# Performance work log

Measured on AMD Instinct MI355X. Metric: run time of the kernel, lower is better.

## Reference

```python
import jax, jax.numpy as jnp
import numpy as np


def setup_inputs() -> dict:
    key = jax.random.key(0)
    k1, k2 = jax.random.split(key)
    imgs = jax.random.normal(k1, (4, 16, 64, 64), dtype=jnp.float32)
    kernel = jax.random.normal(k2, (16, 16, 5, 5), dtype=jnp.float32)
    return {"imgs": imgs, "kernel": kernel, "stride": 1, "padding": 2}


def reference(imgs, kernel, stride, padding):
    # Tropical-max (T+) semifield convolution (morphological dilation):
    #   multiply = add, add_reduce = max, zero = -inf, kind='conv' (kernel flipped)
    B, C, H, W = imgs.shape
    O, _, kH, kW = kernel.shape
    x = jnp.pad(imgs, ((0, 0), (0, 0), (padding, padding), (padding, padding)),
                constant_values=-jnp.inf)
    # kind='conv' flips the kernel spatially
    k = kernel[:, :, ::-1, ::-1]
    # im2col-style window extraction: [B, C*kH*kW, oH, oW], channel-major (C, kH, kW)
    patches = jax.lax.conv_general_dilated_patches(
        x, (kH, kW), (stride, stride), padding="VALID")
    oH, oW = patches.shape[2], patches.shape[3]
    win = patches.reshape(B, 1, C, kH, kW, oH, oW)
    w = k.reshape(1, O, C, kH, kW, 1, 1)
    # broadcast semifield multiply (add), then semifield reduce (max) over (C, kH, kW)
    out = jnp.max(win + w, axis=(2, 3, 4))  # [B, O, oH, oW]
    return out
```

## Files before the change

### kernel.cpp

```cpp
#include <hip/hip_runtime.h>
#include <math.h>


#define NEG_INF (-__builtin_inff())

#define PW 68
#define PPLANE (PW * PW)

__global__ __launch_bounds__(256) void pad_kernel(
        const float* __restrict__ img, float* __restrict__ pad) {
    const int idx   = blockIdx.x * 256 + threadIdx.x;
    const int plane = idx / PPLANE;
    const int rem   = idx % PPLANE;
    const int py    = rem / PW;
    const int px    = rem % PW;
    const int yy = py - 2, xx = px - 2;
    float v = NEG_INF;
    if ((unsigned)yy < 64u && (unsigned)xx < 64u)
        v = img[(plane << 12) + (yy << 6) + xx];
    pad[idx] = v;
}

__global__ __launch_bounds__(256, 4) void bconv_kernel(
        const float* __restrict__ pad,
        const float* __restrict__ kern,
        float* __restrict__ out) {
    const int x  = threadIdx.x & 63;
    const int w  = __builtin_amdgcn_readfirstlane(threadIdx.x >> 6);
    const int y  = blockIdx.x;
    const int og = blockIdx.y;
    const int b  = blockIdx.z;
    const int o0 = og * 4;
    const int c0 = w * 4;

    __shared__ float red[4][4][64];

    float acc0 = NEG_INF, acc1 = NEG_INF, acc2 = NEG_INF, acc3 = NEG_INF;

#pragma unroll
    for (int cc = 0; cc < 4; ++cc) {
        const int c = c0 + cc;
        const float* __restrict__ pl = pad + (b * 16 + c) * PPLANE + y * PW + x;

        float v[25];
#pragma unroll
        for (int i = 0; i < 5; ++i)
#pragma unroll
            for (int j = 0; j < 5; ++j)
                v[i * 5 + j] = pl[i * PW + j];

#define ACC_O(oo, A)                                                     \
        {                                                                \
            const float* __restrict__ kp = kern + ((o0 + oo) * 16 + c) * 25; \
            float kw[25];                                                \
            _Pragma("unroll")                                            \
            for (int t = 0; t < 25; ++t) kw[t] = kp[t];                  \
            _Pragma("unroll")                                            \
            for (int g = 0; g < 5; ++g) {                                \
                float t0 = v[g * 5 + 0] + kw[24 - (g * 5 + 0)];          \
                float t1 = v[g * 5 + 1] + kw[24 - (g * 5 + 1)];          \
                float t2 = v[g * 5 + 2] + kw[24 - (g * 5 + 2)];          \
                float t3 = v[g * 5 + 3] + kw[24 - (g * 5 + 3)];          \
                float t4 = v[g * 5 + 4] + kw[24 - (g * 5 + 4)];          \
                A = fmaxf(A, fmaxf(t0, t1));                             \
                A = fmaxf(A, fmaxf(t2, t3));                             \
                A = fmaxf(A, t4);                                        \
            }                                                            \
        }
        ACC_O(0, acc0)
        ACC_O(1, acc1)
        ACC_O(2, acc2)
        ACC_O(3, acc3)
#undef ACC_O
    }

    red[w][0][x] = acc0;
    red[w][1][x] = acc1;
    red[w][2][x] = acc2;
    red[w][3][x] = acc3;
    __syncthreads();

    const int oo = threadIdx.x >> 6;
    float r = fmaxf(fmaxf(red[0][oo][x], red[1][oo][x]),
                    fmaxf(red[2][oo][x], red[3][oo][x]));
    out[(((b * 16 + o0 + oo) << 6) + y) * 64 + x] = r;
}

extern "C" void kernel_launch(void* const* d_in, const int* in_sizes, int n_in,
                              void* d_out, int out_size, void* d_ws, size_t ws_size,
                              hipStream_t stream) {
    const float* img  = (const float*)d_in[0];
    const float* kern = (const float*)d_in[1];
    float* out = (float*)d_out;
    float* pad = (float*)d_ws;
    (void)in_sizes; (void)n_in; (void)out_size; (void)ws_size;

    hipLaunchKernelGGL(pad_kernel, dim3(1156), dim3(256), 0, stream, img, pad);

    dim3 grid(64, 4, 4);
    hipLaunchKernelGGL(bconv_kernel, grid, dim3(256), 0, stream, pad, kern, out);
}
```

Measured before the change: 66.40 us.

## Vectorize pad and window loads, double block size to 8 channel-split waves

The pad kernel now writes a float4 per thread, so it launches a quarter as many blocks. The conv kernel runs 512 threads with 8 waves, each handling 2 input channels instead of 4, and reduces across 8 partial results in shared memory. Window rows are read with unaligned 4-wide vector loads, the adds use 2-wide vector types, and the channel loop is no longer unrolled. The aim is more parallelism and fewer load instructions, at the cost of a larger reduction and half the threads sitting idle in the final step.

```diff
diff --git a/kernel.cpp b/kernel.cpp
--- a/kernel.cpp
+++ b/kernel.cpp
@@ -3,25 +3,34 @@
 
 
 #define NEG_INF (-__builtin_inff())
-
 #define PW 68
 #define PPLANE (PW * PW)
 
+typedef float f32x2  __attribute__((ext_vector_type(2)));
+typedef float f32x4u __attribute__((ext_vector_type(4), aligned(4)));
+
 __global__ __launch_bounds__(256) void pad_kernel(
         const float* __restrict__ img, float* __restrict__ pad) {
-    const int idx   = blockIdx.x * 256 + threadIdx.x;
-    const int plane = idx / PPLANE;
-    const int rem   = idx % PPLANE;
-    const int py    = rem / PW;
-    const int px    = rem % PW;
-    const int yy = py - 2, xx = px - 2;
-    float v = NEG_INF;
-    if ((unsigned)yy < 64u && (unsigned)xx < 64u)
-        v = img[(plane << 12) + (yy << 6) + xx];
-    pad[idx] = v;
+    const int idx4  = blockIdx.x * 256 + threadIdx.x;
+    const int plane = idx4 / 1156;
+    const int r4    = idx4 - plane * 1156;
+    const int py    = r4 / 17;
+    const int px0   = (r4 - py * 17) * 4;
+    const int yy    = py - 2;
+    const bool yok  = (unsigned)yy < 64u;
+    const float* src = img + (plane << 12) + ((yok ? yy : 0) << 6);
+    float o[4];
+#pragma unroll
+    for (int t = 0; t < 4; ++t) {
+        int xx = px0 + t - 2;
+        bool ok = yok && ((unsigned)xx < 64u);
+        o[t] = ok ? src[(unsigned)xx < 64u ? xx : 0] : NEG_INF;
+    }
+    float4* dst = (float4*)(pad + plane * PPLANE + py * PW + px0);
+    *dst = make_float4(o[0], o[1], o[2], o[3]);
 }
 
-__global__ __launch_bounds__(256, 4) void bconv_kernel(
+__global__ __launch_bounds__(512, 8) void bconv_kernel(
         const float* __restrict__ pad,
         const float* __restrict__ kern,
         float* __restrict__ out) {
@@ -31,41 +40,40 @@
     const int og = blockIdx.y;
     const int b  = blockIdx.z;
     const int o0 = og * 4;
-    const int c0 = w * 4;
+    const int c0 = w * 2;
 
-    __shared__ float red[4][4][64];
+    __shared__ float red[8][4][64];
 
     float acc0 = NEG_INF, acc1 = NEG_INF, acc2 = NEG_INF, acc3 = NEG_INF;
 
-#pragma unroll
-    for (int cc = 0; cc < 4; ++cc) {
+#pragma unroll 1
+    for (int cc = 0; cc < 2; ++cc) {
         const int c = c0 + cc;
         const float* __restrict__ pl = pad + (b * 16 + c) * PPLANE + y * PW + x;
 
-        float v[25];
+        float v[5][5];
 #pragma unroll
-        for (int i = 0; i < 5; ++i)
-#pragma unroll
-            for (int j = 0; j < 5; ++j)
-                v[i * 5 + j] = pl[i * PW + j];
+        for (int i = 0; i < 5; ++i) {
+            f32x4u v4 = *(const f32x4u*)(pl + i * PW);
+            v[i][0] = v4.x; v[i][1] = v4.y; v[i][2] = v4.z; v[i][3] = v4.w;
+            v[i][4] = pl[i * PW + 4];
+        }
 
-#define ACC_O(oo, A)                                                     \
-        {                                                                \
-            const float* __restrict__ kp = kern + ((o0 + oo) * 16 + c) * 25; \
-            float kw[25];                                                \
-            _Pragma("unroll")                                            \
-            for (int t = 0; t < 25; ++t) kw[t] = kp[t];                  \
-            _Pragma("unroll")                                            \
-            for (int g = 0; g < 5; ++g) {                                \
-                float t0 = v[g * 5 + 0] + kw[24 - (g * 5 + 0)];          \
-                float t1 = v[g * 5 + 1] + kw[24 - (g * 5 + 1)];          \
-                float t2 = v[g * 5 + 2] + kw[24 - (g * 5 + 2)];          \
-                float t3 = v[g * 5 + 3] + kw[24 - (g * 5 + 3)];          \
-                float t4 = v[g * 5 + 4] + kw[24 - (g * 5 + 4)];          \
-                A = fmaxf(A, fmaxf(t0, t1));                             \
-                A = fmaxf(A, fmaxf(t2, t3));                             \
-                A = fmaxf(A, t4);                                        \
-            }                                                            \
+#define ACC_O(oo, A)                                                          \
+        {                                                                     \
+            const float* __restrict__ kp = kern + ((o0 + oo) * 16 + c) * 25;  \
+            _Pragma("unroll")                                                 \
+            for (int g = 0; g < 5; ++g) {                                     \
+                const int kb = 24 - g * 5;                                    \
+                f32x2 a01 = (f32x2){v[g][0], v[g][1]}                         \
+                          + (f32x2){kp[kb], kp[kb - 1]};                      \
+                f32x2 a23 = (f32x2){v[g][2], v[g][3]}                         \
+                          + (f32x2){kp[kb - 2], kp[kb - 3]};                  \
+                float a4  = v[g][4] + kp[kb - 4];                             \
+                float m01 = fmaxf(a01.x, a01.y);                              \
+                float m234 = fmaxf(fmaxf(a23.x, a23.y), a4);                  \
+                A = fmaxf(A, fmaxf(m01, m234));                               \
+            }                                                                 \
         }
         ACC_O(0, acc0)
         ACC_O(1, acc1)
@@ -80,10 +88,13 @@
     red[w][3][x] = acc3;
     __syncthreads();
 
-    const int oo = threadIdx.x >> 6;
-    float r = fmaxf(fmaxf(red[0][oo][x], red[1][oo][x]),
-                    fmaxf(red[2][oo][x], red[3][oo][x]));
-    out[(((b * 16 + o0 + oo) << 6) + y) * 64 + x] = r;
+    if (threadIdx.x < 256) {
+        const int oo = threadIdx.x >> 6;
+        float r = red[0][oo][x];
+#pragma unroll
+        for (int ww = 1; ww < 8; ++ww) r = fmaxf(r, red[ww][oo][x]);
+        out[((b * 16 + o0 + oo) << 12) + (y << 6) + x] = r;
+    }
 }
 
 extern "C" void kernel_launch(void* const* d_in, const int* in_sizes, int n_in,
@@ -95,8 +106,8 @@
     float* pad = (float*)d_ws;
     (void)in_sizes; (void)n_in; (void)out_size; (void)ws_size;
 
-    hipLaunchKernelGGL(pad_kernel, dim3(1156), dim3(256), 0, stream, img, pad);
+    hipLaunchKernelGGL(pad_kernel, dim3(289), dim3(256), 0, stream, img, pad);
 
     dim3 grid(64, 4, 4);
-    hipLaunchKernelGGL(bconv_kernel, grid, dim3(256), 0, stream, pad, kern, out);
+    hipLaunchKernelGGL(bconv_kernel, grid, dim3(512), 0, stream, pad, kern, out);
 }
```

New measurement: 65.73 us. About the same (-1.0%).
